# Kernel optimization log

Hardware: AMD Instinct MI355X
Metric: run time of the kernel (lower is better)

## Reference

```python
import jax, jax.numpy as jnp
import numpy as np

N = 50000      # nodes
E = 800000     # edges
D = 128        # d_model
H = 8          # heads
DH = D // H    # head dim
FF = 512       # dim_ff
NB = 32        # degree buckets
EPS = 1e-5


def _ln(x, g, b):
    mu = jnp.mean(x, axis=-1, keepdims=True)
    var = jnp.mean((x - mu) ** 2, axis=-1, keepdims=True)
    return (x - mu) * jax.lax.rsqrt(var + EPS) * g + b


def setup_inputs() -> dict:
    key = jax.random.key(0)
    ks = jax.random.split(key, 12)
    s = 0.02
    return {
        'x': jax.random.normal(ks[0], (N, D), jnp.float32),
        'row': jnp.sort(jax.random.randint(ks[1], (E,), 0, N, jnp.int32)),
        'col': jax.random.randint(ks[2], (E,), 0, N, jnp.int32),
        'deg_bucket': jax.random.randint(ks[3], (N,), 0, NB, jnp.int32),
        'Wq': jax.random.normal(ks[4], (D, D), jnp.float32) * s,
        'bq': jnp.zeros((D,), jnp.float32),
        'Wk': jax.random.normal(ks[5], (D, D), jnp.float32) * s,
        'bk': jnp.zeros((D,), jnp.float32),
        'Wv': jax.random.normal(ks[6], (D, D), jnp.float32) * s,
        'bv': jnp.zeros((D,), jnp.float32),
        'Wo': jax.random.normal(ks[7], (D, D), jnp.float32) * s,
        'bo': jnp.zeros((D,), jnp.float32),
        'emb': jax.random.normal(ks[8], (NB, H), jnp.float32) * s,
        'ln1_g': jnp.ones((D,), jnp.float32), 'ln1_b': jnp.zeros((D,), jnp.float32),
        'ln2_g': jnp.ones((D,), jnp.float32), 'ln2_b': jnp.zeros((D,), jnp.float32),
        'W1': jax.random.normal(ks[9], (D, FF), jnp.float32) * s,
        'b1': jnp.zeros((FF,), jnp.float32),
        'W2': jax.random.normal(ks[10], (FF, D), jnp.float32) * s,
        'b2': jnp.zeros((D,), jnp.float32),
    }


def reference(x, row, col, deg_bucket, Wq, bq, Wk, bk, Wv, bv, Wo, bo, emb,
              ln1_g, ln1_b, ln2_g, ln2_b, W1, b1, W2, b2):
    scale = DH ** (-0.5)
    Q = (x @ Wq + bq).reshape(N, H, DH)
    K = (x @ Wk + bk).reshape(N, H, DH)
    V = (x @ Wv + bv).reshape(N, H, DH)
    # edge-wise QK dot products: [E, H]
    scores = jnp.einsum('ehd,ehd->eh', Q[row], K[col]) * scale
    scores = scores + emb[deg_bucket[row]] + emb[deg_bucket[col]]
    # segment softmax over destination node `row`
    max_s = jax.ops.segment_max(scores, row, num_segments=N, indices_are_sorted=True)
    exp_s = jnp.exp(scores - max_s[row])
    sum_s = jax.ops.segment_sum(exp_s, row, num_segments=N, indices_are_sorted=True)
    alpha = exp_s / jnp.maximum(sum_s[row], 1e-12)
    # scatter-weighted aggregation of V[col]: [N, H, DH]
    agg = jax.ops.segment_sum(alpha[..., None] * V[col], row, num_segments=N,
                              indices_are_sorted=True)
    out = agg.reshape(N, D) @ Wo + bo
    h = _ln(x + out, ln1_g, ln1_b)
    ffo = jax.nn.gelu(h @ W1 + b1, approximate=False) @ W2 + b2
    return _ln(h + ffo, ln2_g, ln2_b)
```

## Files before the change

kernel.cpp:

```cpp
#include <hip/hip_runtime.h>
#include <math.h>

#define NN 50000
#define NE 800000
#define DM 128
#define NH 8
#define FF 512
#define NBLK 391
#define NBLK64 782

#define PB_X    6250
#define PB_WT   192
#define PB_RP   196
#define PB_EMB  1563
#define PB_TOT  (PB_X + PB_WT + PB_RP + PB_EMB)

typedef __attribute__((ext_vector_type(8))) short bf16x8;
typedef __attribute__((ext_vector_type(4))) float f32x4;
typedef __attribute__((ext_vector_type(2))) float f32x2;

__device__ __forceinline__ short f2bf(float f) {
    union { float f; unsigned u; } v; v.f = f;
    unsigned r = v.u + 0x7fff + ((v.u >> 16) & 1);
    return (short)(r >> 16);
}
__device__ __forceinline__ float bf2f(short s) {
    union { unsigned u; float f; } v; v.u = ((unsigned)(unsigned short)s) << 16;
    return v.f;
}
__device__ __forceinline__ unsigned char f2fp8(float f) {
    int p = __builtin_amdgcn_cvt_pk_fp8_f32(f, f, 0, false);
    return (unsigned char)(p & 0xff);
}

__device__ __forceinline__ float gelu_f(float x) {
    float u = x * (0.7978845608f + 0.0356774081f * x * x);
    float t = 1.f - 2.f / (__expf(2.f * u) + 1.f);
    return 0.5f * x * (1.f + t);
}

__device__ __forceinline__ void gload16(const void* g, void* l) {
    __builtin_amdgcn_global_load_lds(
        (const __attribute__((address_space(1))) void*)g,
        (__attribute__((address_space(3))) void*)l, 16, 0, 0);
}

__device__ __forceinline__ void stage_tile(const short* __restrict__ src, int row0,
                                           int maxrow, int ld, int col0,
                                           short* sm) {
    const int tid = threadIdx.x;
    const int w = tid >> 6, l = tid & 63;
    const int p = l & 15;
    #pragma unroll
    for (int j = 0; j < 8; ++j) {
        int lr = w * 32 + j * 4 + (l >> 4);
        int gr = row0 + lr; gr = gr > maxrow ? maxrow : gr;
        int s = p ^ (lr & 7);
        const short* g = src + (size_t)gr * ld + col0 + s * 8;
        gload16(g, sm + (w * 32 + j * 4) * 128);
    }
}

__device__ __forceinline__ void stage_tile64(const short* __restrict__ src, int row0,
                                             int maxrow, int ld, int col0,
                                             short* sm) {
    const int tid = threadIdx.x;
    const int w = tid >> 6, l = tid & 63;
    const int p = l & 15;
    #pragma unroll
    for (int j = 0; j < 4; ++j) {
        int lr = w * 16 + j * 4 + (l >> 4);
        int gr = row0 + lr; gr = gr > maxrow ? maxrow : gr;
        int s = p ^ (lr & 7);
        const short* g = src + (size_t)gr * ld + col0 + s * 8;
        gload16(g, sm + (w * 16 + j * 4) * 128);
    }
}

__device__ __forceinline__ bf16x8 frag_ld(const short* sm, int outer, int slot) {
    return *(const bf16x8*)(sm + outer * 128 + ((slot ^ (outer & 7)) << 3));
}

__device__ __forceinline__ void mfma_tile(const short* sA, const short* sB,
                                          int wm, int wn, int lane,
                                          f32x4 acc[4][4]) {
    const int l15 = lane & 15, l4 = lane >> 4;
    #pragma unroll
    for (int ks = 0; ks < 4; ++ks) {
        bf16x8 a[4], b[4];
        int slot = ks * 4 + l4;
        #pragma unroll
        for (int f = 0; f < 4; ++f) a[f] = frag_ld(sA, wm * 64 + f * 16 + l15, slot);
        #pragma unroll
        for (int f = 0; f < 4; ++f) b[f] = frag_ld(sB, wn * 64 + f * 16 + l15, slot);
        #pragma unroll
        for (int fm = 0; fm < 4; ++fm)
            #pragma unroll
            for (int fn = 0; fn < 4; ++fn)
                acc[fm][fn] = __builtin_amdgcn_mfma_f32_16x16x32_bf16(
                    a[fm], b[fn], acc[fm][fn], 0, 0, 0);
    }
}

__device__ __forceinline__ void mfma_tile64(const short* sA, const short* sB,
                                            int wm, int wn, int lane,
                                            f32x4 acc[2][4]) {
    const int l15 = lane & 15, l4 = lane >> 4;
    #pragma unroll
    for (int ks = 0; ks < 4; ++ks) {
        bf16x8 a[2], b[4];
        int slot = ks * 4 + l4;
        #pragma unroll
        for (int f = 0; f < 2; ++f) a[f] = frag_ld(sA, wm * 32 + f * 16 + l15, slot);
        #pragma unroll
        for (int f = 0; f < 4; ++f) b[f] = frag_ld(sB, wn * 64 + f * 16 + l15, slot);
        #pragma unroll
        for (int fm = 0; fm < 2; ++fm)
            #pragma unroll
            for (int fn = 0; fn < 4; ++fn)
                acc[fm][fn] = __builtin_amdgcn_mfma_f32_16x16x32_bf16(
                    a[fm], b[fn], acc[fm][fn], 0, 0, 0);
    }
}

__global__ __launch_bounds__(256) void k_prep(
    const float* __restrict__ x, short* __restrict__ xb,
    const float* __restrict__ Wq, const float* __restrict__ Wk,
    const float* __restrict__ Wv, const float* __restrict__ Wo,
    const float* __restrict__ W1, const float* __restrict__ W2,
    short* __restrict__ wts,
    const int* __restrict__ row, int* __restrict__ rowptr,
    const int* __restrict__ db, const float* __restrict__ emb,
    float* __restrict__ embn)
{
    int bid = blockIdx.x;
    const int tid = threadIdx.x;

    if (bid < PB_X) {
        int i = bid * 256 + tid;
        if (i < NN * DM / 4) {
            float4 v = ((const float4*)x)[i];
            ((short4*)xb)[i] = make_short4(f2bf(v.x), f2bf(v.y), f2bf(v.z), f2bf(v.w));
        }
        return;
    }
    bid -= PB_X;
    if (bid < PB_WT) {
        const float* W; short* Wt; int K, N, bx, by;
        if (bid < 64) {
            int wsel = bid >> 4, rel = bid & 15;
            W = wsel == 0 ? Wq : wsel == 1 ? Wk : wsel == 2 ? Wv : Wo;
            Wt = wts + wsel * 16384; K = 128; N = 128; bx = rel & 3; by = rel >> 2;
        } else if (bid < 128) {
            int rel = bid - 64;
            W = W1; Wt = wts + 65536; K = 128; N = 512; bx = rel & 15; by = rel >> 4;
        } else {
            int rel = bid - 128;
            W = W2; Wt = wts + 131072; K = 512; N = 128; bx = rel & 3; by = rel >> 2;
        }
        __shared__ float t[32][33];
        int n0 = bx * 32, k0 = by * 32;
        int r = tid >> 3, c4 = (tid & 7) * 4;
        float4 v = *(const float4*)(W + (size_t)(k0 + r) * N + n0 + c4);
        t[r][c4 + 0] = v.x; t[r][c4 + 1] = v.y; t[r][c4 + 2] = v.z; t[r][c4 + 3] = v.w;
        __syncthreads();
        short4 o = make_short4(f2bf(t[c4 + 0][r]), f2bf(t[c4 + 1][r]),
                               f2bf(t[c4 + 2][r]), f2bf(t[c4 + 3][r]));
        *(short4*)(Wt + (size_t)(n0 + r) * K + k0 + c4) = o;
        return;
    }
    bid -= PB_WT;
    if (bid < PB_RP) {
        int n = bid * 256 + tid;
        if (n > NN) return;
        int lo = 0, hi = NE;
        while (lo < hi) {
            int mid = (lo + hi) >> 1;
            if (row[mid] < n) lo = mid + 1; else hi = mid;
        }
        rowptr[n] = lo;
        return;
    }
    bid -= PB_RP;
    {
        int i = bid * 256 + tid;
        if (i < NN * NH) embn[i] = emb[db[i >> 3] * NH + (i & 7)];
    }
}

__global__ __launch_bounds__(256) void k_gemm_qkv(
    const short* __restrict__ xb, const short* __restrict__ Wt,
    const float* __restrict__ bq, const float* __restrict__ bk,
    const float* __restrict__ bv,
    short* __restrict__ Qb, unsigned char* __restrict__ Kf8,
    unsigned char* __restrict__ Vf8)
{
    __shared__ short sm[2 * 16384];
    const int tid = threadIdx.x, lane = tid & 63, wid = tid >> 6;
    const int wm = wid >> 1, wn = wid & 1;
    const int r0 = blockIdx.x * 128;

    stage_tile(xb, r0, NN - 1, 128, 0, sm);
    #pragma unroll
    for (int m = 0; m < 3; ++m) {
        if (m) __syncthreads();
        stage_tile(Wt + m * 16384, 0, 127, 128, 0, sm + 16384);
        __syncthreads();
        f32x4 acc[4][4];
        #pragma unroll
        for (int i = 0; i < 4; ++i)
            #pragma unroll
            for (int j = 0; j < 4; ++j)
                acc[i][j] = (f32x4){0.f, 0.f, 0.f, 0.f};
        mfma_tile(sm, sm + 16384, wm, wn, lane, acc);

        const float* bias = m == 0 ? bq : (m == 1 ? bk : bv);
        #pragma unroll
        for (int fn = 0; fn < 4; ++fn) {
            int col = wn * 64 + fn * 16 + (lane & 15);
            float bc = bias[col];
            #pragma unroll
            for (int fm = 0; fm < 4; ++fm) {
                int rowb = r0 + wm * 64 + fm * 16 + (lane >> 4) * 4;
                #pragma unroll
                for (int rr = 0; rr < 4; ++rr) {
                    int gr = rowb + rr;
                    if (gr < NN) {
                        float v = acc[fm][fn][rr] + bc;
                        if (m == 0)
                            Qb[(size_t)gr * DM + col] = f2bf(v);
                        else if (m == 1)
                            Kf8[(size_t)gr * DM + col] = f2fp8(v);
                        else
                            Vf8[(size_t)gr * DM + col] = f2fp8(v);
                    }
                }
            }
        }
    }
}

__global__ __launch_bounds__(256) void k_attn_wave(
    const short* __restrict__ Qb, const unsigned char* __restrict__ Kf8,
    const unsigned char* __restrict__ Vf8, const int* __restrict__ col,
    const int* __restrict__ rowptr, const float* __restrict__ embn,
    short* __restrict__ aggb)
{
    const int lane = threadIdx.x & 63;
    const int n = blockIdx.x * 4 + (threadIdx.x >> 6);
    const int e0 = rowptr[n], e1 = rowptr[n + 1];
    const int s = lane >> 3, h = lane & 7;
    const int h2 = lane >> 3;

    float qf[16];
    {
        const bf16x8* qp = (const bf16x8*)(Qb + (size_t)n * DM + h * 16);
        bf16x8 q0 = qp[0], q1 = qp[1];
        #pragma unroll
        for (int j = 0; j < 8; ++j) { qf[j] = bf2f(q0[j]); qf[8 + j] = bf2f(q1[j]); }
    }
    const float embr = embn[(size_t)n * NH + h];

    float m = -INFINITY, l = 0.f, acc0 = 0.f, acc1 = 0.f;

    for (int c0 = e0; c0 < e1; c0 += 16) {
        int ea = c0 + s, eb = c0 + 8 + s;
        bool va = ea < e1, vb = eb < e1;
        int ca = col[va ? ea : e1 - 1];
        int cb = col[vb ? eb : e1 - 1];

        int4 kwa = *(const int4*)(Kf8 + (size_t)ca * DM + h * 16);
        int4 kwb = *(const int4*)(Kf8 + (size_t)cb * DM + h * 16);
        float ema = embn[(size_t)ca * NH + h];
        float emB = embn[(size_t)cb * NH + h];

        int nv = e1 - c0; nv = nv > 16 ? 16 : nv;
        unsigned short vv[16];
        #pragma unroll
        for (int j = 0; j < 8; ++j) {
            int cj = __shfl(ca, j * 8);
            vv[j] = (j < nv) ? *(const unsigned short*)(Vf8 + (size_t)cj * DM + lane * 2) : 0;
        }
        #pragma unroll
        for (int j = 0; j < 8; ++j) {
            int cj = __shfl(cb, j * 8);
            vv[8 + j] = (8 + j < nv) ? *(const unsigned short*)(Vf8 + (size_t)cj * DM + lane * 2) : 0;
        }

        float da = 0.f, dbv = 0.f;
        {
            int ka[4] = {kwa.x, kwa.y, kwa.z, kwa.w};
            int kb[4] = {kwb.x, kwb.y, kwb.z, kwb.w};
            #pragma unroll
            for (int w = 0; w < 4; ++w) {
                f32x2 alo = __builtin_amdgcn_cvt_pk_f32_fp8(ka[w], false);
                f32x2 ahi = __builtin_amdgcn_cvt_pk_f32_fp8(ka[w], true);
                f32x2 blo = __builtin_amdgcn_cvt_pk_f32_fp8(kb[w], false);
                f32x2 bhi = __builtin_amdgcn_cvt_pk_f32_fp8(kb[w], true);
                da  += qf[w * 4 + 0] * alo[0] + qf[w * 4 + 1] * alo[1]
                     + qf[w * 4 + 2] * ahi[0] + qf[w * 4 + 3] * ahi[1];
                dbv += qf[w * 4 + 0] * blo[0] + qf[w * 4 + 1] * blo[1]
                     + qf[w * 4 + 2] * bhi[0] + qf[w * 4 + 3] * bhi[1];
            }
        }
        float sa = va ? da * 0.25f + embr + ema : -INFINITY;
        float sb = vb ? dbv * 0.25f + embr + emB : -INFINITY;

        float mc = fmaxf(sa, sb);
        mc = fmaxf(mc, __shfl_xor(mc, 8));
        mc = fmaxf(mc, __shfl_xor(mc, 16));
        mc = fmaxf(mc, __shfl_xor(mc, 32));
        float mn = fmaxf(m, mc);
        float f = __expf(m - mn);
        m = mn;
        float pa = __expf(sa - mn);
        float pb = __expf(sb - mn);
        float ps = pa + pb;
        ps += __shfl_xor(ps, 8);
        ps += __shfl_xor(ps, 16);
        ps += __shfl_xor(ps, 32);
        l = l * f + ps;

        float fr = __shfl(f, h2);
        acc0 *= fr; acc1 *= fr;
        #pragma unroll
        for (int j = 0; j < 8; ++j) {
            float pj = __shfl(pa, j * 8 + h2);
            f32x2 vd = __builtin_amdgcn_cvt_pk_f32_fp8((int)vv[j], false);
            acc0 += pj * vd[0];
            acc1 += pj * vd[1];
        }
        #pragma unroll
        for (int j = 0; j < 8; ++j) {
            float pj = __shfl(pb, j * 8 + h2);
            f32x2 vd = __builtin_amdgcn_cvt_pk_f32_fp8((int)vv[8 + j], false);
            acc0 += pj * vd[0];
            acc1 += pj * vd[1];
        }
    }
    float la = __shfl(l, h2);
    la = fmaxf(la, 1e-12f);
    unsigned o = ((unsigned)(unsigned short)f2bf(acc0 / la)) |
                 (((unsigned)(unsigned short)f2bf(acc1 / la)) << 16);
    *(unsigned*)(aggb + (size_t)n * DM + lane * 2) = o;
}

__global__ __launch_bounds__(256) void k_gemm_ln1(
    const short* __restrict__ aggb, const short* __restrict__ Wot,
    const float* __restrict__ bo, const float* __restrict__ x,
    const float* __restrict__ g, const float* __restrict__ b,
    float* __restrict__ h, short* __restrict__ hb)
{
    __shared__ union { short ab[2 * 16384]; float hs[128 * 129]; } u;
    __shared__ float mu[128], rsd[128];
    const int tid = threadIdx.x, lane = tid & 63, wid = tid >> 6;
    const int wm = wid >> 1, wn = wid & 1;
    const int r0 = blockIdx.x * 128;

    stage_tile(aggb, r0, NN - 1, 128, 0, u.ab);
    stage_tile(Wot, 0, 127, 128, 0, u.ab + 16384);
    __syncthreads();

    f32x4 acc[4][4];
    #pragma unroll
    for (int i = 0; i < 4; ++i)
        #pragma unroll
        for (int j = 0; j < 4; ++j) acc[i][j] = (f32x4){0.f, 0.f, 0.f, 0.f};
    mfma_tile(u.ab, u.ab + 16384, wm, wn, lane, acc);
    __syncthreads();

    #pragma unroll
    for (int fn = 0; fn < 4; ++fn) {
        int col = wn * 64 + fn * 16 + (lane & 15);
        float bc = bo[col];
        #pragma unroll
        for (int fm = 0; fm < 4; ++fm) {
            int rowb = wm * 64 + fm * 16 + (lane >> 4) * 4;
            #pragma unroll
            for (int rr = 0; rr < 4; ++rr) {
                int r_ = rowb + rr, gr = r0 + r_;
                float xr = (gr < NN) ? x[(size_t)gr * DM + col] : 0.f;
                u.hs[r_ * 129 + col] = acc[fm][fn][rr] + bc + xr;
            }
        }
    }
    __syncthreads();

    {
        int rrow = tid >> 1, half = tid & 1;
        float s = 0.f, q = 0.f;
        #pragma unroll 8
        for (int c = 0; c < 64; ++c) {
            float v = u.hs[rrow * 129 + half * 64 + c];
            s += v; q += v * v;
        }
        s += __shfl_xor(s, 1);
        q += __shfl_xor(q, 1);
        float m = s * (1.f / DM);
        float var = q * (1.f / DM) - m * m;
        if (half == 0) { mu[rrow] = m; rsd[rrow] = rsqrtf(var + 1e-5f); }
    }
    __syncthreads();

    for (int i = 0; i < 64; ++i) {
        int idx = i * 256 + tid;
        int rrow = idx >> 7, c = idx & 127;
        int gr = r0 + rrow;
        if (gr < NN) {
            float v = (u.hs[rrow * 129 + c] - mu[rrow]) * rsd[rrow] * g[c] + b[c];
            h[(size_t)gr * DM + c] = v;
            hb[(size_t)gr * DM + c] = f2bf(v);
        }
    }
}

__global__ __launch_bounds__(256) void k_ffn_fused(
    const short* __restrict__ hb, const short* __restrict__ Wt1,
    const float* __restrict__ b1, const short* __restrict__ Wt2,
    const float* __restrict__ b2, const float* __restrict__ h,
    const float* __restrict__ g, const float* __restrict__ bb,
    float* __restrict__ out)
{
    extern __shared__ char smraw[];
    short* A = (short*)smraw;
    short* B = A + 8192;
    short* C = B + 16384;
    float* hs = (float*)smraw;
    __shared__ float mu[64], rsd[64];

    const int tid = threadIdx.x, lane = tid & 63, wid = tid >> 6;
    const int wm = wid >> 1, wn = wid & 1;
    const int r0 = blockIdx.x * 64;

    f32x4 acc2[2][4];
    #pragma unroll
    for (int i = 0; i < 2; ++i)
        #pragma unroll
        for (int j = 0; j < 4; ++j) acc2[i][j] = (f32x4){0.f, 0.f, 0.f, 0.f};

    stage_tile64(hb, r0, NN - 1, 128, 0, A);

    for (int kc = 0; kc < 4; ++kc) {
        if (kc) __syncthreads();
        stage_tile(Wt1, kc * 128, FF - 1, 128, 0, B);
        __syncthreads();

        f32x4 accf[2][4];
        #pragma unroll
        for (int i = 0; i < 2; ++i)
            #pragma unroll
            for (int j = 0; j < 4; ++j) accf[i][j] = (f32x4){0.f, 0.f, 0.f, 0.f};
        mfma_tile64(A, B, wm, wn, lane, accf);

        #pragma unroll
        for (int fn = 0; fn < 4; ++fn) {
            int nloc = wn * 64 + fn * 16 + (lane & 15);
            float bc = b1[kc * 128 + nloc];
            int slot = nloc >> 3;
            #pragma unroll
            for (int fm = 0; fm < 2; ++fm) {
                int rowb = wm * 32 + fm * 16 + (lane >> 4) * 4;
                #pragma unroll
                for (int rr = 0; rr < 4; ++rr) {
                    int row = rowb + rr;
                    float v = gelu_f(accf[fm][fn][rr] + bc);
                    C[row * 128 + (((slot ^ (row & 7)) << 3) | (nloc & 7))] = f2bf(v);
                }
            }
        }
        __syncthreads();
        stage_tile(Wt2, 0, 127, FF, kc * 128, B);
        __syncthreads();
        mfma_tile64(C, B, wm, wn, lane, acc2);
    }
    __syncthreads();

    #pragma unroll
    for (int fn = 0; fn < 4; ++fn) {
        int col = wn * 64 + fn * 16 + (lane & 15);
        float bc = b2[col];
        #pragma unroll
        for (int fm = 0; fm < 2; ++fm) {
            int rowb = wm * 32 + fm * 16 + (lane >> 4) * 4;
            #pragma unroll
            for (int rr = 0; rr < 4; ++rr) {
                int r_ = rowb + rr, gr = r0 + r_;
                float hr = (gr < NN) ? h[(size_t)gr * DM + col] : 0.f;
                hs[r_ * 129 + col] = acc2[fm][fn][rr] + bc + hr;
            }
        }
    }
    __syncthreads();

    {
        int rrow = tid >> 2, q = tid & 3;
        float s = 0.f, qq = 0.f;
        #pragma unroll 8
        for (int c = 0; c < 32; ++c) {
            float v = hs[rrow * 129 + q * 32 + c];
            s += v; qq += v * v;
        }
        s += __shfl_xor(s, 1);  qq += __shfl_xor(qq, 1);
        s += __shfl_xor(s, 2);  qq += __shfl_xor(qq, 2);
        float m = s * (1.f / DM);
        float var = qq * (1.f / DM) - m * m;
        if (q == 0) { mu[rrow] = m; rsd[rrow] = rsqrtf(var + 1e-5f); }
    }
    __syncthreads();

    for (int i = 0; i < 32; ++i) {
        int idx = i * 256 + tid;
        int rrow = idx >> 7, c = idx & 127;
        int gr = r0 + rrow;
        if (gr < NN)
            out[(size_t)gr * DM + c] =
                (hs[rrow * 129 + c] - mu[rrow]) * rsd[rrow] * g[c] + bb[c];
    }
}

extern "C" void kernel_launch(void* const* d_in, const int* in_sizes, int n_in,
                              void* d_out, int out_size, void* d_ws, size_t ws_size,
                              hipStream_t stream) {
    const float* x   = (const float*)d_in[0];
    const int* row   = (const int*)d_in[1];
    const int* col   = (const int*)d_in[2];
    const int* db    = (const int*)d_in[3];
    const float* Wq  = (const float*)d_in[4];
    const float* bq  = (const float*)d_in[5];
    const float* Wk  = (const float*)d_in[6];
    const float* bk  = (const float*)d_in[7];
    const float* Wv  = (const float*)d_in[8];
    const float* bv  = (const float*)d_in[9];
    const float* Wo  = (const float*)d_in[10];
    const float* bo  = (const float*)d_in[11];
    const float* emb = (const float*)d_in[12];
    const float* g1  = (const float*)d_in[13];
    const float* b1n = (const float*)d_in[14];
    const float* g2  = (const float*)d_in[15];
    const float* b2n = (const float*)d_in[16];
    const float* W1  = (const float*)d_in[17];
    const float* b1  = (const float*)d_in[18];
    const float* W2  = (const float*)d_in[19];
    const float* b2  = (const float*)d_in[20];

    char* W = (char*)d_ws;
    float* embn          = (float*)(W + 0);
    unsigned char* Kf8   = (unsigned char*)(W + 1600000);
    unsigned char* Vf8   = (unsigned char*)(W + 8000000);
    short* aggb   = (short*)(W + 25600000);
    short* xb     = (short*)(W + 38400000);
    short* Qb     = (short*)(W + 51200000);
    float* h      = (float*)(W + 51200000);
    short* hb     = (short*)(W + 76800000);
    short* wts    = (short*)(W + 89600000);
    int* rowptr   = (int*)(W + 89993216);

    k_prep<<<PB_TOT, 256, 0, stream>>>(x, xb, Wq, Wk, Wv, Wo, W1, W2, wts,
                                       row, rowptr, db, emb, embn);
    k_gemm_qkv<<<NBLK, 256, 0, stream>>>(xb, wts, bq, bk, bv, Qb, Kf8, Vf8);
    k_attn_wave<<<NN / 4, 256, 0, stream>>>(Qb, Kf8, Vf8, col, rowptr, embn, aggb);
    k_gemm_ln1<<<NBLK, 256, 0, stream>>>(aggb, wts + 49152, bo, x, g1, b1n, h, hb);
    k_ffn_fused<<<NBLK64, 256, 65536, stream>>>(hb, wts + 65536, b1,
                                                wts + 131072, b2, h, g2, b2n,
                                                (float*)d_out);
}
```

Baseline: 208.5 us.

## Run fused FFN GEMMs in FP8 with scaled weights and activations

Converts W1/W2 to FP8 (scaled by 16) in the prep kernel, writes the LN1 output as FP8, and runs both FFN matmuls with fp8 MFMA instructions, rescaling accumulators afterwards. This halves shared-memory staging and global traffic for the FFN operands, lets the dynamic shared allocation shrink, and uses the faster fp8 MFMA rate. The cost is lower precision for h, the GELU intermediate and the weights, which risks exceeding the accuracy tolerance.

```diff
diff --git a/kernel.cpp b/kernel.cpp
--- a/kernel.cpp
+++ b/kernel.cpp
@@ -61,24 +61,31 @@
     }
 }
 
-__device__ __forceinline__ void stage_tile64(const short* __restrict__ src, int row0,
-                                             int maxrow, int ld, int col0,
-                                             short* sm) {
+template <int R>
+__device__ __forceinline__ void stage_tile_f8(const unsigned char* __restrict__ src,
+                                              int row0, int maxrow, int ld, int col0,
+                                              unsigned char* sm) {
     const int tid = threadIdx.x;
     const int w = tid >> 6, l = tid & 63;
-    const int p = l & 15;
-    #pragma unroll
-    for (int j = 0; j < 4; ++j) {
-        int lr = w * 16 + j * 4 + (l >> 4);
+    const int p = l & 7;
+    const int rsub = l >> 3;
+    #pragma unroll
+    for (int j = 0; j < (R >> 5); ++j) {
+        int lr = w * (R >> 2) + j * 8 + rsub;
         int gr = row0 + lr; gr = gr > maxrow ? maxrow : gr;
-        int s = p ^ (lr & 7);
-        const short* g = src + (size_t)gr * ld + col0 + s * 8;
-        gload16(g, sm + (w * 16 + j * 4) * 128);
+        int g = p ^ (lr & 7);
+        const unsigned char* gp = src + (size_t)gr * ld + col0 + g * 16;
+        gload16(gp, sm + (w * (R >> 2) + j * 8) * 128);
     }
 }
 
 __device__ __forceinline__ bf16x8 frag_ld(const short* sm, int outer, int slot) {
     return *(const bf16x8*)(sm + outer * 128 + ((slot ^ (outer & 7)) << 3));
+}
+
+__device__ __forceinline__ long frag_ld_f8(const unsigned char* sm, int outer, int slot) {
+    return *(const long*)(sm + outer * 128 +
+                          (((slot >> 1) ^ (outer & 7)) << 4) + ((slot & 1) << 3));
 }
 
 __device__ __forceinline__ void mfma_tile(const short* sA, const short* sB,
@@ -102,23 +109,24 @@
     }
 }
 
-__device__ __forceinline__ void mfma_tile64(const short* sA, const short* sB,
-                                            int wm, int wn, int lane,
-                                            f32x4 acc[2][4]) {
+__device__ __forceinline__ void mfma_tile64_f8(const unsigned char* sA,
+                                               const unsigned char* sB,
+                                               int wm, int wn, int lane,
+                                               f32x4 acc[2][4]) {
     const int l15 = lane & 15, l4 = lane >> 4;
     #pragma unroll
     for (int ks = 0; ks < 4; ++ks) {
-        bf16x8 a[2], b[4];
+        long a[2], b[4];
         int slot = ks * 4 + l4;
         #pragma unroll
-        for (int f = 0; f < 2; ++f) a[f] = frag_ld(sA, wm * 32 + f * 16 + l15, slot);
-        #pragma unroll
-        for (int f = 0; f < 4; ++f) b[f] = frag_ld(sB, wn * 64 + f * 16 + l15, slot);
+        for (int f = 0; f < 2; ++f) a[f] = frag_ld_f8(sA, wm * 32 + f * 16 + l15, slot);
+        #pragma unroll
+        for (int f = 0; f < 4; ++f) b[f] = frag_ld_f8(sB, wn * 64 + f * 16 + l15, slot);
         #pragma unroll
         for (int fm = 0; fm < 2; ++fm)
             #pragma unroll
             for (int fn = 0; fn < 4; ++fn)
-                acc[fm][fn] = __builtin_amdgcn_mfma_f32_16x16x32_bf16(
+                acc[fm][fn] = __builtin_amdgcn_mfma_f32_16x16x32_fp8_fp8(
                     a[fm], b[fn], acc[fm][fn], 0, 0, 0);
     }
 }
@@ -129,6 +137,7 @@
     const float* __restrict__ Wv, const float* __restrict__ Wo,
     const float* __restrict__ W1, const float* __restrict__ W2,
     short* __restrict__ wts,
+    unsigned char* __restrict__ w1f8, unsigned char* __restrict__ w2f8,
     const int* __restrict__ row, int* __restrict__ rowptr,
     const int* __restrict__ db, const float* __restrict__ emb,
     float* __restrict__ embn)
@@ -146,17 +155,18 @@
     }
     bid -= PB_X;
     if (bid < PB_WT) {
-        const float* W; short* Wt; int K, N, bx, by;
+        const float* W; int K, N, bx, by;
+        short* Wt = nullptr; unsigned char* Wf8 = nullptr;
         if (bid < 64) {
             int wsel = bid >> 4, rel = bid & 15;
             W = wsel == 0 ? Wq : wsel == 1 ? Wk : wsel == 2 ? Wv : Wo;
             Wt = wts + wsel * 16384; K = 128; N = 128; bx = rel & 3; by = rel >> 2;
         } else if (bid < 128) {
             int rel = bid - 64;
-            W = W1; Wt = wts + 65536; K = 128; N = 512; bx = rel & 15; by = rel >> 4;
+            W = W1; Wf8 = w1f8; K = 128; N = 512; bx = rel & 15; by = rel >> 4;
         } else {
             int rel = bid - 128;
-            W = W2; Wt = wts + 131072; K = 512; N = 128; bx = rel & 3; by = rel >> 2;
+            W = W2; Wf8 = w2f8; K = 512; N = 128; bx = rel & 3; by = rel >> 2;
         }
         __shared__ float t[32][33];
         int n0 = bx * 32, k0 = by * 32;
@@ -164,9 +174,15 @@
         float4 v = *(const float4*)(W + (size_t)(k0 + r) * N + n0 + c4);
         t[r][c4 + 0] = v.x; t[r][c4 + 1] = v.y; t[r][c4 + 2] = v.z; t[r][c4 + 3] = v.w;
         __syncthreads();
-        short4 o = make_short4(f2bf(t[c4 + 0][r]), f2bf(t[c4 + 1][r]),
-                               f2bf(t[c4 + 2][r]), f2bf(t[c4 + 3][r]));
-        *(short4*)(Wt + (size_t)(n0 + r) * K + k0 + c4) = o;
+        if (Wt) {
+            short4 o = make_short4(f2bf(t[c4 + 0][r]), f2bf(t[c4 + 1][r]),
+                                   f2bf(t[c4 + 2][r]), f2bf(t[c4 + 3][r]));
+            *(short4*)(Wt + (size_t)(n0 + r) * K + k0 + c4) = o;
+        } else {
+            uchar4 o = make_uchar4(f2fp8(16.f * t[c4 + 0][r]), f2fp8(16.f * t[c4 + 1][r]),
+                                   f2fp8(16.f * t[c4 + 2][r]), f2fp8(16.f * t[c4 + 3][r]));
+            *(uchar4*)(Wf8 + (size_t)(n0 + r) * K + k0 + c4) = o;
+        }
         return;
     }
     bid -= PB_WT;
@@ -349,7 +365,7 @@
     const short* __restrict__ aggb, const short* __restrict__ Wot,
     const float* __restrict__ bo, const float* __restrict__ x,
     const float* __restrict__ g, const float* __restrict__ b,
-    float* __restrict__ h, short* __restrict__ hb)
+    float* __restrict__ h, unsigned char* __restrict__ hb8)
 {
     __shared__ union { short ab[2 * 16384]; float hs[128 * 129]; } u;
     __shared__ float mu[128], rsd[128];
@@ -409,27 +425,28 @@
         if (gr < NN) {
             float v = (u.hs[rrow * 129 + c] - mu[rrow]) * rsd[rrow] * g[c] + b[c];
             h[(size_t)gr * DM + c] = v;
-            hb[(size_t)gr * DM + c] = f2bf(v);
+            hb8[(size_t)gr * DM + c] = f2fp8(v);
         }
     }
 }
 
 __global__ __launch_bounds__(256) void k_ffn_fused(
-    const short* __restrict__ hb, const short* __restrict__ Wt1,
-    const float* __restrict__ b1, const short* __restrict__ Wt2,
+    const unsigned char* __restrict__ hb8, const unsigned char* __restrict__ W1f8,
+    const float* __restrict__ b1, const unsigned char* __restrict__ W2f8,
     const float* __restrict__ b2, const float* __restrict__ h,
     const float* __restrict__ g, const float* __restrict__ bb,
     float* __restrict__ out)
 {
     extern __shared__ char smraw[];
-    short* A = (short*)smraw;
-    short* B = A + 8192;
-    short* C = B + 16384;
+    unsigned char* A = (unsigned char*)smraw;
+    unsigned char* B = A + 8192;
+    unsigned char* C = B + 16384;
     float* hs = (float*)smraw;
     __shared__ float mu[64], rsd[64];
 
     const int tid = threadIdx.x, lane = tid & 63, wid = tid >> 6;
     const int wm = wid >> 1, wn = wid & 1;
+    const int l15 = lane & 15, l4 = lane >> 4;
     const int r0 = blockIdx.x * 64;
 
     f32x4 acc2[2][4];
@@ -438,11 +455,11 @@
         #pragma unroll
         for (int j = 0; j < 4; ++j) acc2[i][j] = (f32x4){0.f, 0.f, 0.f, 0.f};
 
-    stage_tile64(hb, r0, NN - 1, 128, 0, A);
+    stage_tile_f8<64>(hb8, r0, NN - 1, 128, 0, A);
 
     for (int kc = 0; kc < 4; ++kc) {
         if (kc) __syncthreads();
-        stage_tile(Wt1, kc * 128, FF - 1, 128, 0, B);
+        stage_tile_f8<128>(W1f8, kc * 128, FF - 1, 128, 0, B);
         __syncthreads();
 
         f32x4 accf[2][4];
@@ -450,43 +467,43 @@
         for (int i = 0; i < 2; ++i)
             #pragma unroll
             for (int j = 0; j < 4; ++j) accf[i][j] = (f32x4){0.f, 0.f, 0.f, 0.f};
-        mfma_tile64(A, B, wm, wn, lane, accf);
+        mfma_tile64_f8(A, B, wm, wn, lane, accf);
 
         #pragma unroll
         for (int fn = 0; fn < 4; ++fn) {
-            int nloc = wn * 64 + fn * 16 + (lane & 15);
+            int nloc = wn * 64 + fn * 16 + l15;
             float bc = b1[kc * 128 + nloc];
-            int slot = nloc >> 3;
             #pragma unroll
             for (int fm = 0; fm < 2; ++fm) {
-                int rowb = wm * 32 + fm * 16 + (lane >> 4) * 4;
+                int rowb = wm * 32 + fm * 16 + l4 * 4;
                 #pragma unroll
                 for (int rr = 0; rr < 4; ++rr) {
                     int row = rowb + rr;
-                    float v = gelu_f(accf[fm][fn][rr] + bc);
-                    C[row * 128 + (((slot ^ (row & 7)) << 3) | (nloc & 7))] = f2bf(v);
+                    float v = 16.f * gelu_f(accf[fm][fn][rr] * 0.0625f + bc);
+                    C[row * 128 + ((((nloc >> 4) ^ (row & 7)) << 4) | (nloc & 15))]
+                        = f2fp8(v);
                 }
             }
         }
         __syncthreads();
-        stage_tile(Wt2, 0, 127, FF, kc * 128, B);
+        stage_tile_f8<128>(W2f8, 0, 127, 512, kc * 128, B);
         __syncthreads();
-        mfma_tile64(C, B, wm, wn, lane, acc2);
+        mfma_tile64_f8(C, B, wm, wn, lane, acc2);
     }
     __syncthreads();
 
     #pragma unroll
     for (int fn = 0; fn < 4; ++fn) {
-        int col = wn * 64 + fn * 16 + (lane & 15);
+        int col = wn * 64 + fn * 16 + l15;
         float bc = b2[col];
         #pragma unroll
         for (int fm = 0; fm < 2; ++fm) {
-            int rowb = wm * 32 + fm * 16 + (lane >> 4) * 4;
+            int rowb = wm * 32 + fm * 16 + l4 * 4;
             #pragma unroll
             for (int rr = 0; rr < 4; ++rr) {
                 int r_ = rowb + rr, gr = r0 + r_;
                 float hr = (gr < NN) ? h[(size_t)gr * DM + col] : 0.f;
-                hs[r_ * 129 + col] = acc2[fm][fn][rr] + bc + hr;
+                hs[r_ * 129 + col] = acc2[fm][fn][rr] * (1.f / 256.f) + bc + hr;
             }
         }
     }
@@ -551,16 +568,17 @@
     short* xb     = (short*)(W + 38400000);
     short* Qb     = (short*)(W + 51200000);
     float* h      = (float*)(W + 51200000);
-    short* hb     = (short*)(W + 76800000);
+    unsigned char* hb8 = (unsigned char*)(W + 76800000);
     short* wts    = (short*)(W + 89600000);
-    int* rowptr   = (int*)(W + 89993216);
+    unsigned char* w1f8 = (unsigned char*)(W + 89731072);
+    unsigned char* w2f8 = (unsigned char*)(W + 89796608);
+    int* rowptr   = (int*)(W + 89862144);
 
     k_prep<<<PB_TOT, 256, 0, stream>>>(x, xb, Wq, Wk, Wv, Wo, W1, W2, wts,
-                                       row, rowptr, db, emb, embn);
+                                       w1f8, w2f8, row, rowptr, db, emb, embn);
     k_gemm_qkv<<<NBLK, 256, 0, stream>>>(xb, wts, bq, bk, bv, Qb, Kf8, Vf8);
     k_attn_wave<<<NN / 4, 256, 0, stream>>>(Qb, Kf8, Vf8, col, rowptr, embn, aggb);
-    k_gemm_ln1<<<NBLK, 256, 0, stream>>>(aggb, wts + 49152, bo, x, g1, b1n, h, hb);
-    k_ffn_fused<<<NBLK64, 256, 65536, stream>>>(hb, wts + 65536, b1,
-                                                wts + 131072, b2, h, g2, b2n,
-                                                (float*)d_out);
-}
+    k_gemm_ln1<<<NBLK, 256, 0, stream>>>(aggb, wts + 49152, bo, x, g1, b1n, h, hb8);
+    k_ffn_fused<<<NBLK64, 256, 33024, stream>>>(hb8, w1f8, b1, w2f8, b2, h,
+                                                g2, b2n, (float*)d_out);
+}
```

Measured after the change: 203.9 us. -2.2%, faster.
